# Optimization experiments

Hardware: AMD Instinct MI355X
Metric: run time of the kernel (lower is better)

## Reference

```python
import math
import jax, jax.numpy as jnp
import numpy as np

B, S, D, H = 2, 2048, 1024, 16
HD = D // H
I = 3752  # round(1024 * 11/3 / 8) * 8, per GluMLP default
EPS = 1e-6


def _alibi_bias(nheads, n):
    # AlibiPostionEmbedding: slopes (power-of-2 formula) * -1, times |i-j|
    start = 2.0 ** (-(2.0 ** (-(math.log2(nheads) - 3))))
    slopes = np.array([start * start ** i for i in range(nheads)], dtype=np.float64) * -1.0
    pos = np.arange(n)
    rel = np.abs(pos[None, :] - pos[:, None])  # [n, n]
    return jnp.asarray(slopes[:, None, None] * rel[None, :, :], dtype=jnp.float32)


def rmsnorm(h, w):
    h32 = h.astype(jnp.float32)
    var = jnp.mean(h32 * h32, axis=-1, keepdims=True)
    return (w * (h32 * jax.lax.rsqrt(var + EPS))).astype(h.dtype)


def setup_inputs() -> dict:
    key = jax.random.key(0)
    ks = jax.random.split(key, 16)
    sd = 1.0 / math.sqrt(D)
    si = 1.0 / math.sqrt(I)
    rn = lambda k, shape, s: jax.random.normal(k, shape, jnp.float32) * s
    return {
        "x": rn(ks[0], (B, S, D), 1.0),
        "wq": rn(ks[1], (D, D), sd), "bq": rn(ks[2], (D,), 0.02),
        "wk": rn(ks[3], (D, D), sd), "bk": rn(ks[4], (D,), 0.02),
        "wv": rn(ks[5], (D, D), sd), "bv": rn(ks[6], (D,), 0.02),
        "wo": rn(ks[7], (D, D), sd), "bo": rn(ks[8], (D,), 0.02),
        "w_gate": rn(ks[9], (D, I), sd),
        "w_up": rn(ks[10], (D, I), sd),
        "w_down": rn(ks[11], (I, D), si),
        "ln1_w": jnp.ones((D,), jnp.float32),
        "ln2_w": jnp.ones((D,), jnp.float32),
        "attn_bias": _alibi_bias(H, S),                       # [H, S, S]
        "tgt_mask": jnp.triu(jnp.ones((S, S), bool), 1),      # causal, True = masked
        "key_padding_mask": jnp.zeros((B, S), bool),          # True = padded
    }


def reference(x, wq, bq, wk, bk, wv, bv, wo, bo, w_gate, w_up, w_down,
              ln1_w, ln2_w, attn_bias, tgt_mask, key_padding_mask):
    # ---- TransformerEncoderLayer.forward (eval mode: dropout = identity) ----
    residual = x
    h = rmsnorm(x, ln1_w)
    # MultiheadAttention with ALiBi bias + fused bool masks
    q = (h @ wq + bq).reshape(B, S, H, HD)
    k = (h @ wk + bk).reshape(B, S, H, HD)
    v = (h @ wv + bv).reshape(B, S, H, HD)
    scores = jnp.einsum("bqhd,bkhd->bhqk", q, k) * (HD ** -0.5)  # [B,H,S,S]
    scores = scores + attn_bias[None]
    mask = tgt_mask[None, :, :] | key_padding_mask[:, None, :]   # [B,S,S]
    scores = jnp.where(mask[:, None, :, :], -jnp.inf, scores)
    probs = jax.nn.softmax(scores, axis=-1)
    attn = jnp.einsum("bhqk,bkhd->bqhd", probs, v).reshape(B, S, D)
    attn = attn @ wo + bo
    residual = attn + residual
    # GluMLP (SwiGLU)
    h2 = rmsnorm(residual, ln2_w)
    mlp = (jax.nn.silu(h2 @ w_gate) * (h2 @ w_up)) @ w_down
    return mlp + residual
```

## Files before the change

### kernel.cpp

```cpp
#include <hip/hip_runtime.h>
#include <hip/hip_bf16.h>
#include <cmath>

typedef __bf16 bf16_t;
typedef __bf16 bf16x8 __attribute__((ext_vector_type(8)));
typedef short  s16x8  __attribute__((ext_vector_type(8)));
typedef float  f32x4  __attribute__((ext_vector_type(4)));

static constexpr int Bn  = 2;
static constexpr int Sn  = 2048;
static constexpr int Dn  = 1024;
static constexpr int Hn  = 16;
static constexpr int In  = 3752;
static constexpr int Mn  = Bn * Sn;
static constexpr int Ipad = 3840;

__device__ __forceinline__ void cp16(const bf16_t* g, bf16_t* l) {
  __builtin_amdgcn_global_load_lds(
      (const __attribute__((address_space(1))) unsigned int*)g,
      (__attribute__((address_space(3))) unsigned int*)l, 16, 0, 0);
}

__device__ __forceinline__ void xcd_map(int bid, int nM, int nN, int& m, int& n) {
  const int q = (nM * nN) >> 3;
  const int L = (bid & 7) * q + (bid >> 3);
  const int bandw = nN << 3;
  const int band = L / bandw;
  const int rem  = L - band * bandw;
  n = rem >> 3;
  m = (band << 3) + (rem & 7);
}

struct TransJob  { const float* src; bf16_t* dst; int R, C, bx, start; };
struct TransJobs { TransJob j[7]; };

__global__ __launch_bounds__(256) void k_transpose_all(TransJobs jobs) {
  const int bid = blockIdx.x;
  int jj = 0;
#pragma unroll
  for (int t = 1; t < 7; ++t)
    if (bid >= jobs.j[t].start) jj = t;
  const TransJob jb = jobs.j[jj];
  const int local = bid - jb.start;
  const int r0 = (local / jb.bx) * 32, c0 = (local % jb.bx) * 32;
  __shared__ float tile[32][33];
  const int tx = threadIdx.x & 31, ty = threadIdx.x >> 5;
#pragma unroll
  for (int e = 0; e < 4; ++e) {
    int r = r0 + ty + e * 8, c = c0 + tx;
    if (r < jb.R && c < jb.C) tile[ty + e * 8][tx] = jb.src[(size_t)r * jb.C + c];
  }
  __syncthreads();
#pragma unroll
  for (int e = 0; e < 4; ++e) {
    int c = c0 + ty + e * 8, r = r0 + tx;
    if (r < jb.R && c < jb.C) jb.dst[(size_t)c * jb.R + r] = (bf16_t)tile[tx][ty + e * 8];
  }
}

__global__ __launch_bounds__(256) void k_rmsnorm(const float* __restrict__ in,
                                                 const float* __restrict__ w,
                                                 bf16_t* __restrict__ out) {
  const int row = blockIdx.x;
  const int tid = threadIdx.x;
  const float* ip = in + (size_t)row * Dn;
  float v[4];
  float ss = 0.f;
#pragma unroll
  for (int e = 0; e < 4; ++e) {
    v[e] = ip[tid + e * 256];
    ss += v[e] * v[e];
  }
  for (int off = 32; off > 0; off >>= 1) ss += __shfl_down(ss, off);
  __shared__ float red[4];
  if ((tid & 63) == 0) red[tid >> 6] = ss;
  __syncthreads();
  float tot = red[0] + red[1] + red[2] + red[3];
  float sc = rsqrtf(tot * (1.0f / Dn) + 1e-6f);
  bf16_t* op = out + (size_t)row * Dn;
#pragma unroll
  for (int e = 0; e < 4; ++e) {
    int idx = tid + e * 256;
    op[idx] = (bf16_t)(w[idx] * v[e] * sc);
  }
}

template <int MODE>
__global__ __launch_bounds__(512, 2) void k_gemm256(
    const bf16_t* __restrict__ A, const bf16_t* __restrict__ Bt,
    const float* __restrict__ b0, const float* __restrict__ b1,
    const float* __restrict__ b2,
    bf16_t* __restrict__ out, int ldo, int Nb) {
  __shared__ bf16_t As[3][256 * 32];
  __shared__ bf16_t Bs[3][256 * 32];
  const int m0 = blockIdx.x * 256, n0 = blockIdx.y * 256;
  const int tid = threadIdx.x;
  const int lane = tid & 63, w = tid >> 6;
  const int wm = w >> 2, wn = w & 3;
  const int l15 = lane & 15, quad = lane >> 4;
  const int sw2 = (l15 >> 1) & 3;
  const int slr = lane >> 2, slc = lane & 3;

  int arow[2], brow[2], chk[2], slab[2];
#pragma unroll
  for (int c = 0; c < 2; ++c) {
    const int r = (w * 2 + c) * 16 + slr;
    arow[c] = m0 + r;
    brow[c] = min(n0 + r, Nb - 1);
    chk[c]  = (slc ^ ((r >> 1) & 3)) * 8;
    slab[c] = (w * 2 + c) * 512;
  }

  f32x4 acc[8][4];
  const f32x4 z4 = {0.f, 0.f, 0.f, 0.f};
#pragma unroll
  for (int i = 0; i < 8; ++i)
#pragma unroll
    for (int j = 0; j < 4; ++j) acc[i][j] = z4;

  constexpr int NT = Dn / 32;

  auto stage = [&](int t) {
    const int bi = t - (t / 3) * 3;
    const int k0 = t * 32;
#pragma unroll
    for (int c = 0; c < 2; ++c) {
      cp16(A  + (size_t)arow[c] * Dn + k0 + chk[c], &As[bi][slab[c]]);
      cp16(Bt + (size_t)brow[c] * Dn + k0 + chk[c], &Bs[bi][slab[c]]);
    }
  };

  stage(0);
  stage(1);
  asm volatile("s_waitcnt vmcnt(4)" ::: "memory");
  asm volatile("s_barrier" ::: "memory");

  for (int t = 0; t < NT; ++t) {
    const int bi = t - (t / 3) * 3;
    if (t + 2 < NT) stage(t + 2);

    bf16x8 af[8], bfr[4];
#pragma unroll
    for (int j = 0; j < 4; ++j) {
      const int r2 = wn * 64 + j * 16 + l15;
      bfr[j] = *(const bf16x8*)(&Bs[bi][r2 * 32 + ((quad ^ sw2) * 8)]);
    }
#pragma unroll
    for (int i = 0; i < 8; ++i) {
      const int r2 = wm * 128 + i * 16 + l15;
      af[i] = *(const bf16x8*)(&As[bi][r2 * 32 + ((quad ^ sw2) * 8)]);
    }
    __builtin_amdgcn_s_setprio(1);
#pragma unroll
    for (int i = 0; i < 8; ++i)
#pragma unroll
      for (int j = 0; j < 4; ++j)
        acc[i][j] = __builtin_amdgcn_mfma_f32_16x16x32_bf16(af[i], bfr[j], acc[i][j], 0, 0, 0);
    __builtin_amdgcn_s_setprio(0);

    if (t + 2 < NT) asm volatile("s_waitcnt vmcnt(4)" ::: "memory");
    else            asm volatile("s_waitcnt vmcnt(0)" ::: "memory");
    asm volatile("s_barrier" ::: "memory");
  }

#pragma unroll
  for (int i = 0; i < 8; ++i)
#pragma unroll
    for (int j = 0; j < 4; ++j) {
      const int col = n0 + wn * 64 + j * 16 + l15;
      float bval = 0.f;
      if (MODE == 0) {
        const int sel = col >> 10;
        bval = (sel == 0) ? b0[col] : (sel == 1) ? b1[col - 1024] : b2[col - 2048];
      }
#pragma unroll
      for (int r = 0; r < 4; ++r) {
        const int row = m0 + wm * 128 + i * 16 + quad * 4 + r;
        out[(size_t)row * ldo + col] = (bf16_t)(acc[i][j][r] + bval);
      }
    }
}

__global__ __launch_bounds__(256, 2) void k_gateup(
    const bf16_t* __restrict__ A, const bf16_t* __restrict__ Bg,
    const bf16_t* __restrict__ Bu, bf16_t* __restrict__ out) {
  __shared__ bf16_t As[3][128 * 32];
  __shared__ bf16_t Gs[3][128 * 32];
  __shared__ bf16_t Us[3][128 * 32];
  const int m0 = blockIdx.x * 128, n0 = blockIdx.y * 128;
  const int tid = threadIdx.x;
  const int lane = tid & 63, w = tid >> 6;
  const int wm = w >> 1, wn = w & 1;
  const int l15 = lane & 15, quad = lane >> 4;
  const int sw2 = (l15 >> 1) & 3;

  int arow[2], brow[2], chk[2], slab[2];
#pragma unroll
  for (int c = 0; c < 2; ++c) {
    const int r = (tid >> 2) + 64 * c;
    arow[c] = m0 + r;
    brow[c] = min(n0 + r, In - 1);
    chk[c]  = ((tid & 3) ^ ((r >> 1) & 3)) * 8;
    slab[c] = c * 2048 + w * 512;
  }

  f32x4 accg[4][4], accu[4][4];
  const f32x4 z4 = {0.f, 0.f, 0.f, 0.f};
#pragma unroll
  for (int i = 0; i < 4; ++i)
#pragma unroll
    for (int j = 0; j < 4; ++j) { accg[i][j] = z4; accu[i][j] = z4; }

  constexpr int NT = Dn / 32;

  auto stage = [&](int t) {
    const int bi = t - (t / 3) * 3;
    const int k0 = t * 32;
#pragma unroll
    for (int c = 0; c < 2; ++c) {
      cp16(A  + (size_t)arow[c] * Dn + k0 + chk[c], &As[bi][slab[c]]);
      cp16(Bg + (size_t)brow[c] * Dn + k0 + chk[c], &Gs[bi][slab[c]]);
      cp16(Bu + (size_t)brow[c] * Dn + k0 + chk[c], &Us[bi][slab[c]]);
    }
  };

  stage(0);
  stage(1);
  asm volatile("s_waitcnt vmcnt(6)" ::: "memory");
  asm volatile("s_barrier" ::: "memory");

  for (int t = 0; t < NT; ++t) {
    const int bi = t - (t / 3) * 3;
    if (t + 2 < NT) stage(t + 2);

    bf16x8 af[4], gf[4], uf[4];
#pragma unroll
    for (int i = 0; i < 4; ++i) {
      const int r2 = wm * 64 + i * 16 + l15;
      af[i] = *(const bf16x8*)(&As[bi][r2 * 32 + ((quad ^ sw2) * 8)]);
    }
#pragma unroll
    for (int j = 0; j < 4; ++j) {
      const int r2 = wn * 64 + j * 16 + l15;
      gf[j] = *(const bf16x8*)(&Gs[bi][r2 * 32 + ((quad ^ sw2) * 8)]);
      uf[j] = *(const bf16x8*)(&Us[bi][r2 * 32 + ((quad ^ sw2) * 8)]);
    }
    __builtin_amdgcn_s_setprio(1);
#pragma unroll
    for (int i = 0; i < 4; ++i)
#pragma unroll
      for (int j = 0; j < 4; ++j) {
        accg[i][j] = __builtin_amdgcn_mfma_f32_16x16x32_bf16(af[i], gf[j], accg[i][j], 0, 0, 0);
        accu[i][j] = __builtin_amdgcn_mfma_f32_16x16x32_bf16(af[i], uf[j], accu[i][j], 0, 0, 0);
      }
    __builtin_amdgcn_s_setprio(0);

    if (t + 2 < NT) asm volatile("s_waitcnt vmcnt(6)" ::: "memory");
    else            asm volatile("s_waitcnt vmcnt(0)" ::: "memory");
    asm volatile("s_barrier" ::: "memory");
  }

#pragma unroll
  for (int i = 0; i < 4; ++i)
#pragma unroll
    for (int j = 0; j < 4; ++j) {
      const int col = n0 + wn * 64 + j * 16 + l15;
#pragma unroll
      for (int r = 0; r < 4; ++r) {
        const int row = m0 + wm * 64 + i * 16 + quad * 4 + r;
        const float g = accg[i][j][r];
        const float u = accu[i][j][r];
        const float sl = g / (1.f + expf(-g));
        out[(size_t)row * Ipad + col] = (col < In) ? (bf16_t)(sl * u) : (bf16_t)0.f;
      }
    }
}

__global__ __launch_bounds__(256) void k_gemm64(
    const bf16_t* __restrict__ A, const bf16_t* __restrict__ Bt,
    const float* __restrict__ bias, const float* __restrict__ resid,
    float* __restrict__ outf, int N, int K, int lda, int ldb, int nN) {
  __shared__ bf16_t As[64 * 64];
  __shared__ bf16_t Bs[128 * 64];
  int mblk, nblk;
  xcd_map(blockIdx.x, Mn / 64, nN, mblk, nblk);
  const int m0 = mblk * 64, n0 = nblk * 128;
  const int tid = threadIdx.x;
  const int lane = tid & 63, wid = tid >> 6;
  const int wc = wid * 32;
  const int l15 = lane & 15, quad = lane >> 4;
  const int sw = l15 & 7;
  const int srow_lo = lane >> 3, pchunk = lane & 7;

  f32x4 acc[4][2];
  const f32x4 z4 = {0.f, 0.f, 0.f, 0.f};
#pragma unroll
  for (int i = 0; i < 4; ++i)
#pragma unroll
    for (int j = 0; j < 2; ++j) acc[i][j] = z4;

  for (int k0 = 0; k0 < K; k0 += 64) {
#pragma unroll
    for (int c = 0; c < 2; ++c) {
      const int r = (wid * 2 + c) * 8 + srow_lo;
      const int gc = pchunk ^ (r & 7);
      cp16(A + (size_t)(m0 + r) * lda + k0 + gc * 8, As + (wid * 2 + c) * 512);
    }
#pragma unroll
    for (int c = 0; c < 4; ++c) {
      const int r = (wid * 4 + c) * 8 + srow_lo;
      const int gc = pchunk ^ (r & 7);
      cp16(Bt + (size_t)(n0 + r) * ldb + k0 + gc * 8, Bs + (wid * 4 + c) * 512);
    }
    __syncthreads();
#pragma unroll
    for (int kh = 0; kh < 2; ++kh) {
      const int ph = ((kh * 4 + quad) ^ sw) * 8;
      bf16x8 af[4], bfr[2];
#pragma unroll
      for (int i = 0; i < 4; ++i)
        af[i] = *(const bf16x8*)(As + (i * 16 + l15) * 64 + ph);
#pragma unroll
      for (int j = 0; j < 2; ++j)
        bfr[j] = *(const bf16x8*)(Bs + (wc + j * 16 + l15) * 64 + ph);
#pragma unroll
      for (int i = 0; i < 4; ++i)
#pragma unroll
        for (int j = 0; j < 2; ++j)
          acc[i][j] = __builtin_amdgcn_mfma_f32_16x16x32_bf16(af[i], bfr[j], acc[i][j], 0, 0, 0);
    }
    __syncthreads();
  }

#pragma unroll
  for (int i = 0; i < 4; ++i)
#pragma unroll
    for (int j = 0; j < 2; ++j) {
      const int col = n0 + wc + j * 16 + l15;
      const float bval = bias ? bias[col] : 0.f;
#pragma unroll
      for (int r = 0; r < 4; ++r) {
        const int row = m0 + i * 16 + quad * 4 + r;
        const size_t idx = (size_t)row * N + col;
        outf[idx] = acc[i][j][r] + bval + (resid ? resid[idx] : 0.f);
      }
    }
}

__global__ __launch_bounds__(256) void k_attn(
    const bf16_t* __restrict__ qkv, bf16_t* __restrict__ Ob) {
  const int qt = (int)gridDim.x - 1 - (int)blockIdx.x;
  const int h  = blockIdx.y;
  const int b  = blockIdx.z;
  constexpr int LDK = 72, LDP = 76;
  __shared__ bf16_t Ks[64 * LDK];
  __shared__ bf16_t Vt[64 * LDK];
  __shared__ bf16_t Ps[4][32 * LDP];

  const int tid  = threadIdx.x;
  const int lane = tid & 63, w = tid >> 6;
  const int l15  = lane & 15, quad = lane >> 4;

  constexpr float L2E = 1.4426950408889634f;
  const float slopeL = -exp2f(-0.5f * (float)(h + 1)) * L2E;

  bf16x8 aq[2][2];
#pragma unroll
  for (int g = 0; g < 2; ++g) {
    const int row = qt * 128 + w * 32 + g * 16 + l15;
    const bf16_t* qp = qkv + (size_t)(b * Sn + row) * 3072 + h * 64;
    aq[g][0] = *(const bf16x8*)(qp + quad * 8);
    aq[g][1] = *(const bf16x8*)(qp + 32 + quad * 8);
#pragma unroll
    for (int e = 0; e < 8; ++e) {
      aq[g][0][e] = (bf16_t)((float)aq[g][0][e] * 0.125f);
      aq[g][1][e] = (bf16_t)((float)aq[g][1][e] * 0.125f);
    }
  }

  int qrow[2];
  float rowterm[2][4];
#pragma unroll
  for (int g = 0; g < 2; ++g) {
    qrow[g] = qt * 128 + w * 32 + g * 16 + quad * 4;
#pragma unroll
    for (int rr = 0; rr < 4; ++rr) rowterm[g][rr] = slopeL * (float)(qrow[g] + rr);
  }
  float colbase[4];
#pragma unroll
  for (int t = 0; t < 4; ++t) colbase[t] = slopeL * (float)(t * 16 + l15);

  f32x4 o[2][4], lacc[2];
  const f32x4 z4 = {0.f, 0.f, 0.f, 0.f};
#pragma unroll
  for (int g = 0; g < 2; ++g) {
    lacc[g] = z4;
#pragma unroll
    for (int dt = 0; dt < 4; ++dt) o[g][dt] = z4;
  }
  bf16x8 ones;
#pragma unroll
  for (int e = 0; e < 8; ++e) ones[e] = (bf16_t)1.0f;

  const int r = tid >> 2, c0e = (tid & 3) * 16;
  const size_t kbase = (size_t)(b * Sn + r) * 3072 + 1024 + h * 64 + c0e;
  const size_t step  = (size_t)64 * 3072;

  s16x8 kr0 = *(const s16x8*)(qkv + kbase);
  s16x8 kr1 = *(const s16x8*)(qkv + kbase + 8);
  s16x8 vr0 = *(const s16x8*)(qkv + kbase + 1024);
  s16x8 vr1 = *(const s16x8*)(qkv + kbase + 1024 + 8);

  const int nkt = 2 * qt + 2;
  for (int kt = 0; kt < nkt; ++kt) {
    __syncthreads();
    *(s16x8*)(Ks + r * LDK + c0e)     = kr0;
    *(s16x8*)(Ks + r * LDK + c0e + 8) = kr1;
    {
      const bf16x8 v0 = *(const bf16x8*)&vr0, v1 = *(const bf16x8*)&vr1;
#pragma unroll
      for (int e = 0; e < 8; ++e) {
        Vt[(c0e + e) * LDK + r]     = v0[e];
        Vt[(c0e + 8 + e) * LDK + r] = v1[e];
      }
    }
    __syncthreads();
    if (kt + 1 < nkt) {
      const size_t kb = kbase + (size_t)(kt + 1) * step;
      kr0 = *(const s16x8*)(qkv + kb);
      kr1 = *(const s16x8*)(qkv + kb + 8);
      vr0 = *(const s16x8*)(qkv + kb + 1024);
      vr1 = *(const s16x8*)(qkv + kb + 1024 + 8);
    }

    const float kofs = slopeL * (float)(kt * 64);
    const bool diag = (kt + 2 >= nkt);

#pragma unroll
    for (int g = 0; g < 2; ++g) {
      f32x4 s[4];
#pragma unroll
      for (int t = 0; t < 4; ++t) s[t] = z4;
#pragma unroll
      for (int t = 0; t < 4; ++t) {
        bf16x8 bk0 = *(const bf16x8*)(Ks + (t * 16 + l15) * LDK + quad * 8);
        bf16x8 bk1 = *(const bf16x8*)(Ks + (t * 16 + l15) * LDK + 32 + quad * 8);
        s[t] = __builtin_amdgcn_mfma_f32_16x16x32_bf16(aq[g][0], bk0, s[t], 0, 0, 0);
        s[t] = __builtin_amdgcn_mfma_f32_16x16x32_bf16(aq[g][1], bk1, s[t], 0, 0, 0);
      }
#pragma unroll
      for (int t = 0; t < 4; ++t) {
        const int j = kt * 64 + t * 16 + l15;
#pragma unroll
        for (int rr = 0; rr < 4; ++rr) {
          float v2 = fmaf(s[t][rr], L2E, rowterm[g][rr] - (kofs + colbase[t]));
          if (diag && j > qrow[g] + rr) v2 = -3.0e38f;
          Ps[w][(g * 16 + quad * 4 + rr) * LDP + t * 16 + l15] = (bf16_t)exp2f(v2);
        }
      }
    }

#pragma unroll
    for (int g = 0; g < 2; ++g) {
#pragma unroll
      for (int kh = 0; kh < 2; ++kh) {
        bf16x8 pa = *(const bf16x8*)(Ps[w] + (g * 16 + l15) * LDP + kh * 32 + quad * 8);
        lacc[g] = __builtin_amdgcn_mfma_f32_16x16x32_bf16(pa, ones, lacc[g], 0, 0, 0);
#pragma unroll
        for (int dt = 0; dt < 4; ++dt) {
          bf16x8 bv = *(const bf16x8*)(Vt + (dt * 16 + l15) * LDK + kh * 32 + quad * 8);
          o[g][dt] = __builtin_amdgcn_mfma_f32_16x16x32_bf16(pa, bv, o[g][dt], 0, 0, 0);
        }
      }
    }
  }

#pragma unroll
  for (int g = 0; g < 2; ++g)
#pragma unroll
    for (int rr = 0; rr < 4; ++rr) {
      const float inv = 1.f / lacc[g][rr];
      bf16_t* op = Ob + (size_t)(b * Sn + qrow[g] + rr) * 1024 + h * 64;
#pragma unroll
      for (int dt = 0; dt < 4; ++dt)
        op[dt * 16 + l15] = (bf16_t)(o[g][dt][rr] * inv);
    }
}

extern "C" void kernel_launch(void* const* d_in, const int* in_sizes, int n_in,
                              void* d_out, int out_size, void* d_ws, size_t ws_size,
                              hipStream_t stream) {
  (void)in_sizes; (void)n_in; (void)out_size; (void)ws_size;
  const float* x   = (const float*)d_in[0];
  const float* wq  = (const float*)d_in[1];
  const float* bq  = (const float*)d_in[2];
  const float* wk_ = (const float*)d_in[3];
  const float* bk  = (const float*)d_in[4];
  const float* wv  = (const float*)d_in[5];
  const float* bv  = (const float*)d_in[6];
  const float* wo  = (const float*)d_in[7];
  const float* bo  = (const float*)d_in[8];
  const float* wg  = (const float*)d_in[9];
  const float* wu  = (const float*)d_in[10];
  const float* wd  = (const float*)d_in[11];
  const float* ln1 = (const float*)d_in[12];
  const float* ln2 = (const float*)d_in[13];

  char* base = (char*)d_ws;
  const size_t MiB = 1024 * 1024;
  bf16_t* h1    = (bf16_t*)(base);
  bf16_t* wqkvT = (bf16_t*)(base + 8   * MiB);
  bf16_t* woT   = (bf16_t*)(base + 16  * MiB);
  bf16_t* wgT   = (bf16_t*)(base + 24  * MiB);
  bf16_t* wuT   = (bf16_t*)(base + 32  * MiB);
  bf16_t* wdT   = (bf16_t*)(base + 40  * MiB);
  bf16_t* qkvb  = (bf16_t*)(base + 48  * MiB);
  float*  res1  = (float*) (base + 72  * MiB);
  bf16_t* mlp   = (bf16_t*)(base + 88  * MiB);
  bf16_t* attnb = (bf16_t*)d_out;
  bf16_t* h2    = (bf16_t*)d_out;

  const dim3 blk(256);
  const dim3 blk512(512);

  TransJobs jobs;
  int start = 0;
  auto setjob = [&](int idx, const float* s, bf16_t* d, int R, int C) {
    const int bx = (C + 31) / 32, by = (R + 31) / 32;
    jobs.j[idx] = {s, d, R, C, bx, start};
    start += bx * by;
  };
  setjob(0, wq,  wqkvT,                       Dn, Dn);
  setjob(1, wk_, wqkvT + (size_t)Dn * Dn,     Dn, Dn);
  setjob(2, wv,  wqkvT + 2 * (size_t)Dn * Dn, Dn, Dn);
  setjob(3, wo,  woT, Dn, Dn);
  setjob(4, wg,  wgT, Dn, In);
  setjob(5, wu,  wuT, Dn, In);
  setjob(6, wd,  wdT, In, Dn);
  k_transpose_all<<<dim3(start), blk, 0, stream>>>(jobs);

  k_rmsnorm<<<dim3(Mn), blk, 0, stream>>>(x, ln1, h1);

  k_gemm256<0><<<dim3(Mn / 256, 3072 / 256), blk512, 0, stream>>>(
      h1, wqkvT, bq, bk, bv, qkvb, 3072, 3072);

  k_attn<<<dim3(Sn / 128, Hn, Bn), blk, 0, stream>>>(qkvb, attnb);

  k_gemm64<<<dim3((Mn / 64) * (Dn / 128)), blk, 0, stream>>>(
      attnb, woT, bo, x, res1, Dn, Dn, Dn, Dn, Dn / 128);

  k_rmsnorm<<<dim3(Mn), blk, 0, stream>>>(res1, ln2, h2);

  k_gateup<<<dim3(Mn / 128, Ipad / 128), blk, 0, stream>>>(h2, wgT, wuT, mlp);

  k_gemm64<<<dim3((Mn / 64) * (Dn / 128)), blk, 0, stream>>>(
      mlp, wdT, nullptr, res1, (float*)d_out, Dn, Ipad, Ipad, In, Dn / 128);
}
```

Baseline: 693.1 us.

## Replace 64x128 output GEMM with 128x128 triple-buffered pipelined GEMM

```diff
diff --git a/kernel.cpp b/kernel.cpp
--- a/kernel.cpp
+++ b/kernel.cpp
@@ -19,16 +19,6 @@
   __builtin_amdgcn_global_load_lds(
       (const __attribute__((address_space(1))) unsigned int*)g,
       (__attribute__((address_space(3))) unsigned int*)l, 16, 0, 0);
-}
-
-__device__ __forceinline__ void xcd_map(int bid, int nM, int nN, int& m, int& n) {
-  const int q = (nM * nN) >> 3;
-  const int L = (bid & 7) * q + (bid >> 3);
-  const int bandw = nN << 3;
-  const int band = L / bandw;
-  const int rem  = L - band * bandw;
-  n = rem >> 3;
-  m = (band << 3) + (rem & 7);
 }
 
 struct TransJob  { const float* src; bf16_t* dst; int R, C, bx, start; };
@@ -276,71 +266,90 @@
     }
 }
 
-__global__ __launch_bounds__(256) void k_gemm64(
+__global__ __launch_bounds__(256, 2) void k_gemm128f(
     const bf16_t* __restrict__ A, const bf16_t* __restrict__ Bt,
     const float* __restrict__ bias, const float* __restrict__ resid,
-    float* __restrict__ outf, int N, int K, int lda, int ldb, int nN) {
-  __shared__ bf16_t As[64 * 64];
-  __shared__ bf16_t Bs[128 * 64];
-  int mblk, nblk;
-  xcd_map(blockIdx.x, Mn / 64, nN, mblk, nblk);
-  const int m0 = mblk * 64, n0 = nblk * 128;
+    float* __restrict__ outf, int N, int K, int lda, int ldb) {
+  __shared__ bf16_t As[3][128 * 32];
+  __shared__ bf16_t Bs[3][128 * 32];
+  const int m0 = blockIdx.x * 128, n0 = blockIdx.y * 128;
   const int tid = threadIdx.x;
-  const int lane = tid & 63, wid = tid >> 6;
-  const int wc = wid * 32;
+  const int lane = tid & 63, w = tid >> 6;
+  const int wm = w >> 1, wn = w & 1;
   const int l15 = lane & 15, quad = lane >> 4;
-  const int sw = l15 & 7;
-  const int srow_lo = lane >> 3, pchunk = lane & 7;
-
-  f32x4 acc[4][2];
+  const int sw2 = (l15 >> 1) & 3;
+
+  int arow[2], brow[2], chk[2], slab[2];
+#pragma unroll
+  for (int c = 0; c < 2; ++c) {
+    const int r = (tid >> 2) + 64 * c;
+    arow[c] = m0 + r;
+    brow[c] = n0 + r;
+    chk[c]  = ((tid & 3) ^ ((r >> 1) & 3)) * 8;
+    slab[c] = c * 2048 + w * 512;
+  }
+
+  f32x4 acc[4][4];
   const f32x4 z4 = {0.f, 0.f, 0.f, 0.f};
 #pragma unroll
   for (int i = 0; i < 4; ++i)
 #pragma unroll
-    for (int j = 0; j < 2; ++j) acc[i][j] = z4;
-
-  for (int k0 = 0; k0 < K; k0 += 64) {
+    for (int j = 0; j < 4; ++j) acc[i][j] = z4;
+
+  const int NT = K / 32;
+
+  auto stage = [&](int t) {
+    const int bi = t - (t / 3) * 3;
+    const int k0 = t * 32;
 #pragma unroll
     for (int c = 0; c < 2; ++c) {
-      const int r = (wid * 2 + c) * 8 + srow_lo;
-      const int gc = pchunk ^ (r & 7);
-      cp16(A + (size_t)(m0 + r) * lda + k0 + gc * 8, As + (wid * 2 + c) * 512);
-    }
-#pragma unroll
-    for (int c = 0; c < 4; ++c) {
-      const int r = (wid * 4 + c) * 8 + srow_lo;
-      const int gc = pchunk ^ (r & 7);
-      cp16(Bt + (size_t)(n0 + r) * ldb + k0 + gc * 8, Bs + (wid * 4 + c) * 512);
-    }
-    __syncthreads();
-#pragma unroll
-    for (int kh = 0; kh < 2; ++kh) {
-      const int ph = ((kh * 4 + quad) ^ sw) * 8;
-      bf16x8 af[4], bfr[2];
-#pragma unroll
-      for (int i = 0; i < 4; ++i)
-        af[i] = *(const bf16x8*)(As + (i * 16 + l15) * 64 + ph);
-#pragma unroll
-      for (int j = 0; j < 2; ++j)
-        bfr[j] = *(const bf16x8*)(Bs + (wc + j * 16 + l15) * 64 + ph);
-#pragma unroll
-      for (int i = 0; i < 4; ++i)
-#pragma unroll
-        for (int j = 0; j < 2; ++j)
-          acc[i][j] = __builtin_amdgcn_mfma_f32_16x16x32_bf16(af[i], bfr[j], acc[i][j], 0, 0, 0);
-    }
-    __syncthreads();
+      cp16(A  + (size_t)arow[c] * lda + k0 + chk[c], &As[bi][slab[c]]);
+      cp16(Bt + (size_t)brow[c] * ldb + k0 + chk[c], &Bs[bi][slab[c]]);
+    }
+  };
+
+  stage(0);
+  stage(1);
+  asm volatile("s_waitcnt vmcnt(4)" ::: "memory");
+  asm volatile("s_barrier" ::: "memory");
+
+  for (int t = 0; t < NT; ++t) {
+    const int bi = t - (t / 3) * 3;
+    if (t + 2 < NT) stage(t + 2);
+
+    bf16x8 af[4], bfr[4];
+#pragma unroll
+    for (int i = 0; i < 4; ++i) {
+      const int r2 = wm * 64 + i * 16 + l15;
+      af[i] = *(const bf16x8*)(&As[bi][r2 * 32 + ((quad ^ sw2) * 8)]);
+    }
+#pragma unroll
+    for (int j = 0; j < 4; ++j) {
+      const int r2 = wn * 64 + j * 16 + l15;
+      bfr[j] = *(const bf16x8*)(&Bs[bi][r2 * 32 + ((quad ^ sw2) * 8)]);
+    }
+    __builtin_amdgcn_s_setprio(1);
+#pragma unroll
+    for (int i = 0; i < 4; ++i)
+#pragma unroll
+      for (int j = 0; j < 4; ++j)
+        acc[i][j] = __builtin_amdgcn_mfma_f32_16x16x32_bf16(af[i], bfr[j], acc[i][j], 0, 0, 0);
+    __builtin_amdgcn_s_setprio(0);
+
+    if (t + 2 < NT) asm volatile("s_waitcnt vmcnt(4)" ::: "memory");
+    else            asm volatile("s_waitcnt vmcnt(0)" ::: "memory");
+    asm volatile("s_barrier" ::: "memory");
   }
 
 #pragma unroll
   for (int i = 0; i < 4; ++i)
 #pragma unroll
-    for (int j = 0; j < 2; ++j) {
-      const int col = n0 + wc + j * 16 + l15;
+    for (int j = 0; j < 4; ++j) {
+      const int col = n0 + wn * 64 + j * 16 + l15;
       const float bval = bias ? bias[col] : 0.f;
 #pragma unroll
       for (int r = 0; r < 4; ++r) {
-        const int row = m0 + i * 16 + quad * 4 + r;
+        const int row = m0 + wm * 64 + i * 16 + quad * 4 + r;
         const size_t idx = (size_t)row * N + col;
         outf[idx] = acc[i][j][r] + bval + (resid ? resid[idx] : 0.f);
       }
@@ -546,13 +555,13 @@
 
   k_attn<<<dim3(Sn / 128, Hn, Bn), blk, 0, stream>>>(qkvb, attnb);
 
-  k_gemm64<<<dim3((Mn / 64) * (Dn / 128)), blk, 0, stream>>>(
-      attnb, woT, bo, x, res1, Dn, Dn, Dn, Dn, Dn / 128);
+  k_gemm128f<<<dim3(Mn / 128, Dn / 128), blk, 0, stream>>>(
+      attnb, woT, bo, x, res1, Dn, Dn, Dn, Dn);
 
   k_rmsnorm<<<dim3(Mn), blk, 0, stream>>>(res1, ln2, h2);
 
   k_gateup<<<dim3(Mn / 128, Ipad / 128), blk, 0, stream>>>(h2, wgT, wuT, mlp);
 
-  k_gemm64<<<dim3((Mn / 64) * (Dn / 128)), blk, 0, stream>>>(
-      mlp, wdT, nullptr, res1, (float*)d_out, Dn, Ipad, Ipad, In, Dn / 128);
-}
+  k_gemm128f<<<dim3(Mn / 128, Dn / 128), blk, 0, stream>>>(
+      mlp, wdT, nullptr, res1, (float*)d_out, Dn, Ipad, Ipad, In);
+}
```

Result: slower. 747.2 us (+7.8%).

## Retile QKV GEMM to 256x128 and use split-K big-tile GEMM for down projection

Applied to the files above, without the earlier changes.

```diff
diff --git a/kernel.cpp b/kernel.cpp
--- a/kernel.cpp
+++ b/kernel.cpp
@@ -86,29 +86,28 @@
 }
 
 template <int MODE>
-__global__ __launch_bounds__(512, 2) void k_gemm256(
+__global__ __launch_bounds__(256, 2) void k_gemm256x128(
     const bf16_t* __restrict__ A, const bf16_t* __restrict__ Bt,
     const float* __restrict__ b0, const float* __restrict__ b1,
-    const float* __restrict__ b2,
-    bf16_t* __restrict__ out, int ldo, int Nb) {
+    const float* __restrict__ b2, void* __restrict__ outv,
+    int lda, int ldb) {
   __shared__ bf16_t As[3][256 * 32];
-  __shared__ bf16_t Bs[3][256 * 32];
-  const int m0 = blockIdx.x * 256, n0 = blockIdx.y * 256;
+  __shared__ bf16_t Bs[3][128 * 32];
+  const int m0 = blockIdx.x * 256, n0 = blockIdx.y * 128;
+  const int kbase = (MODE == 1) ? (int)blockIdx.z * (Ipad / 2) : 0;
   const int tid = threadIdx.x;
   const int lane = tid & 63, w = tid >> 6;
-  const int wm = w >> 2, wn = w & 3;
+  const int wm = w >> 1, wn = w & 1;
   const int l15 = lane & 15, quad = lane >> 4;
   const int sw2 = (l15 >> 1) & 3;
-  const int slr = lane >> 2, slc = lane & 3;
-
-  int arow[2], brow[2], chk[2], slab[2];
-#pragma unroll
-  for (int c = 0; c < 2; ++c) {
-    const int r = (w * 2 + c) * 16 + slr;
-    arow[c] = m0 + r;
-    brow[c] = min(n0 + r, Nb - 1);
-    chk[c]  = (slc ^ ((r >> 1) & 3)) * 8;
-    slab[c] = (w * 2 + c) * 512;
+
+  int arow[4], achk[4], aslab[4];
+#pragma unroll
+  for (int c = 0; c < 4; ++c) {
+    const int r = (tid >> 2) + 64 * c;
+    arow[c]  = r;
+    achk[c]  = ((tid & 3) ^ ((r >> 1) & 3)) * 8;
+    aslab[c] = c * 2048 + w * 512;
   }
 
   f32x4 acc[8][4];
@@ -118,21 +117,22 @@
 #pragma unroll
     for (int j = 0; j < 4; ++j) acc[i][j] = z4;
 
-  constexpr int NT = Dn / 32;
+  const int NT = (MODE == 1) ? (Ipad / 2) / 32 : Dn / 32;
 
   auto stage = [&](int t) {
     const int bi = t - (t / 3) * 3;
-    const int k0 = t * 32;
-#pragma unroll
-    for (int c = 0; c < 2; ++c) {
-      cp16(A  + (size_t)arow[c] * Dn + k0 + chk[c], &As[bi][slab[c]]);
-      cp16(Bt + (size_t)brow[c] * Dn + k0 + chk[c], &Bs[bi][slab[c]]);
-    }
+    const int k0 = kbase + t * 32;
+#pragma unroll
+    for (int c = 0; c < 4; ++c)
+      cp16(A + (size_t)(m0 + arow[c]) * lda + k0 + achk[c], &As[bi][aslab[c]]);
+#pragma unroll
+    for (int c = 0; c < 2; ++c)
+      cp16(Bt + (size_t)(n0 + arow[c]) * ldb + k0 + achk[c], &Bs[bi][aslab[c]]);
   };
 
   stage(0);
   stage(1);
-  asm volatile("s_waitcnt vmcnt(4)" ::: "memory");
+  asm volatile("s_waitcnt vmcnt(6)" ::: "memory");
   asm volatile("s_barrier" ::: "memory");
 
   for (int t = 0; t < NT; ++t) {
@@ -141,15 +141,15 @@
 
     bf16x8 af[8], bfr[4];
 #pragma unroll
+    for (int i = 0; i < 8; ++i) {
+      const int r2 = wm * 128 + i * 16 + l15;
+      af[i] = *(const bf16x8*)(&As[bi][r2 * 32 + ((quad ^ sw2) * 8)]);
+    }
+#pragma unroll
     for (int j = 0; j < 4; ++j) {
       const int r2 = wn * 64 + j * 16 + l15;
       bfr[j] = *(const bf16x8*)(&Bs[bi][r2 * 32 + ((quad ^ sw2) * 8)]);
     }
-#pragma unroll
-    for (int i = 0; i < 8; ++i) {
-      const int r2 = wm * 128 + i * 16 + l15;
-      af[i] = *(const bf16x8*)(&As[bi][r2 * 32 + ((quad ^ sw2) * 8)]);
-    }
     __builtin_amdgcn_s_setprio(1);
 #pragma unroll
     for (int i = 0; i < 8; ++i)
@@ -158,7 +158,7 @@
         acc[i][j] = __builtin_amdgcn_mfma_f32_16x16x32_bf16(af[i], bfr[j], acc[i][j], 0, 0, 0);
     __builtin_amdgcn_s_setprio(0);
 
-    if (t + 2 < NT) asm volatile("s_waitcnt vmcnt(4)" ::: "memory");
+    if (t + 2 < NT) asm volatile("s_waitcnt vmcnt(6)" ::: "memory");
     else            asm volatile("s_waitcnt vmcnt(0)" ::: "memory");
     asm volatile("s_barrier" ::: "memory");
   }
@@ -168,17 +168,37 @@
 #pragma unroll
     for (int j = 0; j < 4; ++j) {
       const int col = n0 + wn * 64 + j * 16 + l15;
-      float bval = 0.f;
       if (MODE == 0) {
         const int sel = col >> 10;
-        bval = (sel == 0) ? b0[col] : (sel == 1) ? b1[col - 1024] : b2[col - 2048];
-      }
-#pragma unroll
-      for (int r = 0; r < 4; ++r) {
-        const int row = m0 + wm * 128 + i * 16 + quad * 4 + r;
-        out[(size_t)row * ldo + col] = (bf16_t)(acc[i][j][r] + bval);
-      }
-    }
+        const float bval = (sel == 0) ? b0[col] : (sel == 1) ? b1[col - 1024] : b2[col - 2048];
+        bf16_t* out = (bf16_t*)outv;
+#pragma unroll
+        for (int r = 0; r < 4; ++r) {
+          const int row = m0 + wm * 128 + i * 16 + quad * 4 + r;
+          out[(size_t)row * 3072 + col] = (bf16_t)(acc[i][j][r] + bval);
+        }
+      } else {
+        float* outp = (float*)outv + (size_t)blockIdx.z * Mn * Dn;
+#pragma unroll
+        for (int r = 0; r < 4; ++r) {
+          const int row = m0 + wm * 128 + i * 16 + quad * 4 + r;
+          outp[(size_t)row * Dn + col] = acc[i][j][r];
+        }
+      }
+    }
+}
+
+__global__ __launch_bounds__(256) void k_combine(
+    const float* __restrict__ a, const float* __restrict__ b,
+    const float* __restrict__ c, float* __restrict__ out) {
+  const size_t i = ((size_t)blockIdx.x * 256 + threadIdx.x) * 4;
+  const f32x4 va = *(const f32x4*)(a + i);
+  const f32x4 vb = *(const f32x4*)(b + i);
+  const f32x4 vc = *(const f32x4*)(c + i);
+  f32x4 vo;
+#pragma unroll
+  for (int e = 0; e < 4; ++e) vo[e] = va[e] + vb[e] + vc[e];
+  *(f32x4*)(out + i) = vo;
 }
 
 __global__ __launch_bounds__(256, 2) void k_gateup(
@@ -517,11 +537,11 @@
   bf16_t* qkvb  = (bf16_t*)(base + 48  * MiB);
   float*  res1  = (float*) (base + 72  * MiB);
   bf16_t* mlp   = (bf16_t*)(base + 88  * MiB);
+  float*  parts = (float*) (base + 120 * MiB);
   bf16_t* attnb = (bf16_t*)d_out;
   bf16_t* h2    = (bf16_t*)d_out;
 
   const dim3 blk(256);
-  const dim3 blk512(512);
 
   TransJobs jobs;
   int start = 0;
@@ -541,8 +561,8 @@
 
   k_rmsnorm<<<dim3(Mn), blk, 0, stream>>>(x, ln1, h1);
 
-  k_gemm256<0><<<dim3(Mn / 256, 3072 / 256), blk512, 0, stream>>>(
-      h1, wqkvT, bq, bk, bv, qkvb, 3072, 3072);
+  k_gemm256x128<0><<<dim3(Mn / 256, 3072 / 128), blk, 0, stream>>>(
+      h1, wqkvT, bq, bk, bv, qkvb, Dn, Dn);
 
   k_attn<<<dim3(Sn / 128, Hn, Bn), blk, 0, stream>>>(qkvb, attnb);
 
@@ -553,6 +573,9 @@
 
   k_gateup<<<dim3(Mn / 128, Ipad / 128), blk, 0, stream>>>(h2, wgT, wuT, mlp);
 
-  k_gemm64<<<dim3((Mn / 64) * (Dn / 128)), blk, 0, stream>>>(
-      mlp, wdT, nullptr, res1, (float*)d_out, Dn, Ipad, Ipad, In, Dn / 128);
-}
+  k_gemm256x128<1><<<dim3(Mn / 256, Dn / 128, 2), blk, 0, stream>>>(
+      mlp, wdT, nullptr, nullptr, nullptr, parts, Ipad, In);
+
+  k_combine<<<dim3((Mn * Dn) / 1024), blk, 0, stream>>>(
+      parts, parts + (size_t)Mn * Dn, res1, (float*)d_out);
+}
```

After: 700.4 us. Within noise of the previous version (+1.0%).
